# Kernel optimization log

Hardware: AMD Instinct MI355X
Metric: run time of the kernel (lower is better)

Reference implementation:

```python
import jax, jax.numpy as jnp
import numpy as np

N = 100000
E = 1600000
G = 64  # number of graphs
EPS = 1e-5
NEG_SLOPE = 0.2


def _gat_conv(x, W, a_src, a_dst, b, src, dst, n, H, C):
    # x: [n, in]; W: [in, H*C]; a_src/a_dst: [H, C]; b: [H*C]
    h = (x @ W).reshape(n, H, C)                      # [n,H,C]
    al_s = jnp.sum(h * a_src, axis=-1)                # [n,H]
    al_d = jnp.sum(h * a_dst, axis=-1)                # [n,H]
    score = jax.nn.leaky_relu(al_s[src] + al_d[dst], NEG_SLOPE)  # [E,H]
    # segment softmax over incoming edges of each dst node
    m = jax.ops.segment_max(score, dst, num_segments=n)
    ex = jnp.exp(score - jax.lax.stop_gradient(m)[dst])
    den = jax.ops.segment_sum(ex, dst, num_segments=n)
    alpha = ex / den[dst]                             # [E,H]
    out = jax.ops.segment_sum(alpha[:, :, None] * h[src], dst, num_segments=n)
    return out.reshape(n, H * C) + b


def _bn_relu(x, gamma, beta):
    mu = jnp.mean(x, axis=0)
    var = jnp.var(x, axis=0)  # biased, matches torch BN normalization
    return jax.nn.relu((x - mu) * jax.lax.rsqrt(var + EPS) * gamma + beta)


def setup_inputs() -> dict:
    key = jax.random.key(0)
    ks = jax.random.split(key, 32)
    d = {}
    d['x'] = jax.random.normal(ks[0], (N, 3), dtype=jnp.float32)
    d['edge_index'] = jax.random.randint(ks[1], (2, E), 0, N, dtype=jnp.int64)
    d['batch'] = jnp.sort(jax.random.randint(ks[2], (N,), 0, G, dtype=jnp.int64))
    def p(k, shape):
        return jax.random.normal(k, shape, dtype=jnp.float32) * 0.1
    # conv1: 3 -> 16, heads=2
    d['W1'] = p(ks[3], (3, 32)); d['as1'] = p(ks[4], (2, 16)); d['ad1'] = p(ks[5], (2, 16)); d['b1'] = p(ks[6], (32,))
    d['g1'] = jnp.ones((32,), jnp.float32); d['be1'] = jnp.zeros((32,), jnp.float32)
    # conv2: 32 -> 32, heads=2
    d['W2'] = p(ks[7], (32, 64)); d['as2'] = p(ks[8], (2, 32)); d['ad2'] = p(ks[9], (2, 32)); d['b2'] = p(ks[10], (64,))
    d['g2'] = jnp.ones((64,), jnp.float32); d['be2'] = jnp.zeros((64,), jnp.float32)
    # conv3: 64 -> 64, heads=2
    d['W3'] = p(ks[11], (64, 128)); d['as3'] = p(ks[12], (2, 64)); d['ad3'] = p(ks[13], (2, 64)); d['b3'] = p(ks[14], (128,))
    d['g3'] = jnp.ones((128,), jnp.float32); d['be3'] = jnp.zeros((128,), jnp.float32)
    d['fcw'] = p(ks[15], (128, 10)); d['fcb'] = p(ks[16], (10,))
    return d


def reference(x, edge_index, batch, W1, as1, ad1, b1, g1, be1, W2, as2, ad2, b2, g2, be2, W3, as3, ad3, b3, g3, be3, fcw, fcb):
    n = x.shape[0]
    loops = jnp.arange(n, dtype=edge_index.dtype)  # PyG GATConv add_self_loops=True
    src = jnp.concatenate([edge_index[0], loops])
    dst = jnp.concatenate([edge_index[1], loops])
    h = _bn_relu(_gat_conv(x, W1, as1, ad1, b1, src, dst, n, 2, 16), g1, be1)
    h = _bn_relu(_gat_conv(h, W2, as2, ad2, b2, src, dst, n, 2, 32), g2, be2)
    h = _bn_relu(_gat_conv(h, W3, as3, ad3, b3, src, dst, n, 2, 64), g3, be3)
    pooled = jax.ops.segment_max(h, batch, num_segments=G)  # [G,128]
    return pooled @ fcw + fcb
```

## Files before the change

kernel.cpp:

```cpp
#include <hip/hip_runtime.h>
#include <cstddef>

constexpr int NN = 100000;
constexpr int NE = 1600000;
constexpr int TE = NE + NN;
constexpr int NG = 64;
constexpr float EPS = 1e-5f;
constexpr float NEG_SLOPE = 0.2f;
constexpr int NREP = 16;

constexpr int NBUCK = 256;
constexpr int DPB = 391;
constexpr int PHB = 256;
constexpr int CH = (TE + PHB - 1) / PHB;

__device__ __forceinline__ unsigned short f2bf(float f) {
    unsigned u = __float_as_uint(f);
    u += 0x7fffu + ((u >> 16) & 1u);
    return (unsigned short)(u >> 16);
}
__device__ __forceinline__ float bf2f(unsigned short s) {
    return __uint_as_float((unsigned)s << 16);
}
__device__ __forceinline__ float bflo(unsigned u) { return __uint_as_float(u << 16); }
__device__ __forceinline__ float bfhi(unsigned u) { return __uint_as_float(u & 0xffff0000u); }
__device__ __forceinline__ void unpack8(uint4 v, float* f) {
    f[0] = bflo(v.x); f[1] = bfhi(v.x); f[2] = bflo(v.y); f[3] = bfhi(v.y);
    f[4] = bflo(v.z); f[5] = bfhi(v.z); f[6] = bflo(v.w); f[7] = bfhi(v.w);
}
__device__ __forceinline__ uint4 pack8(const float* o) {
    uint4 pk;
    pk.x = (unsigned)f2bf(o[0]) | ((unsigned)f2bf(o[1]) << 16);
    pk.y = (unsigned)f2bf(o[2]) | ((unsigned)f2bf(o[3]) << 16);
    pk.z = (unsigned)f2bf(o[4]) | ((unsigned)f2bf(o[5]) << 16);
    pk.w = (unsigned)f2bf(o[6]) | ((unsigned)f2bf(o[7]) << 16);
    return pk;
}
__device__ __forceinline__ float lrelu(float v) { return v > 0.f ? v : NEG_SLOPE * v; }


__global__ void k_hist(const int* __restrict__ ei, int* __restrict__ hist) {
    __shared__ int hcnt[NBUCK];
    for (int i = threadIdx.x; i < NBUCK; i += 256) hcnt[i] = 0;
    __syncthreads();
    int k = blockIdx.x;
    int e0 = k * CH, e1 = min(e0 + CH, TE);
    for (int e = e0 + threadIdx.x; e < e1; e += 256) {
        int d = (e < NE) ? ei[NE + e] : (e - NE);
        atomicAdd(&hcnt[d / DPB], 1);
    }
    __syncthreads();
    for (int b = threadIdx.x; b < NBUCK; b += 256) hist[b * PHB + k] = hcnt[b];
}

__global__ void k_scanA(int* __restrict__ hist, int* __restrict__ bsum) {
    __shared__ int ls[PHB];
    int b = blockIdx.x, t = threadIdx.x;
    int v = hist[b * PHB + t];
    ls[t] = v;
    __syncthreads();
    for (int off = 1; off < PHB; off <<= 1) {
        int add = (t >= off) ? ls[t - off] : 0;
        __syncthreads();
        ls[t] += add;
        __syncthreads();
    }
    hist[b * PHB + t] = ls[t] - v;
    if (t == PHB - 1) bsum[b] = ls[t];
}

__global__ void k_scanB(const int* __restrict__ bsum, int* __restrict__ bbase,
                        int* __restrict__ rowptr) {
    __shared__ int ls[NBUCK];
    int t = threadIdx.x;
    int v = bsum[t];
    ls[t] = v;
    __syncthreads();
    for (int off = 1; off < NBUCK; off <<= 1) {
        int add = (t >= off) ? ls[t - off] : 0;
        __syncthreads();
        ls[t] += add;
        __syncthreads();
    }
    bbase[t] = ls[t] - v;
    if (t == NBUCK - 1) { bbase[NBUCK] = ls[t]; rowptr[NN] = ls[t]; }
}

__global__ void k_scatter(const int* __restrict__ ei, const int* __restrict__ hist,
                          const int* __restrict__ bbase, int* __restrict__ pairs) {
    __shared__ int cur[NBUCK];
    int k = blockIdx.x;
    for (int b = threadIdx.x; b < NBUCK; b += 256) cur[b] = bbase[b] + hist[b * PHB + k];
    __syncthreads();
    int e0 = k * CH, e1 = min(e0 + CH, TE);
    for (int e = e0 + threadIdx.x; e < e1; e += 256) {
        int s, d;
        if (e < NE) { s = ei[e]; d = ei[NE + e]; } else { s = e - NE; d = s; }
        int b = d / DPB, ld = d - b * DPB;
        int pos = atomicAdd(&cur[b], 1);
        pairs[pos] = (s << 9) | ld;
    }
}

__global__ void k_csr(const int* __restrict__ pairs, const int* __restrict__ bbase,
                      int* __restrict__ rowptr, int* __restrict__ colsrc) {
    __shared__ int deg[DPB];
    __shared__ int exc[DPB];
    __shared__ int sc[512];
    int b = blockIdx.x, t = threadIdx.x;
    int base = bbase[b], cnt = bbase[b + 1] - base;
    int d0 = b * DPB;
    int ndst = min(DPB, NN - d0);
    for (int i = t; i < DPB; i += 256) deg[i] = 0;
    __syncthreads();
    for (int i = t; i < cnt; i += 256) atomicAdd(&deg[pairs[base + i] & 511], 1);
    __syncthreads();
    sc[t] = (t < DPB) ? deg[t] : 0;
    sc[t + 256] = (t + 256 < DPB) ? deg[t + 256] : 0;
    __syncthreads();
    for (int off = 1; off < 512; off <<= 1) {
        int a0 = (t >= off) ? sc[t - off] : 0;
        int a1 = (t + 256 >= off) ? sc[t + 256 - off] : 0;
        __syncthreads();
        sc[t] += a0; sc[t + 256] += a1;
        __syncthreads();
    }
    if (t < DPB) exc[t] = sc[t] - deg[t];
    if (t + 256 < DPB) exc[t + 256] = sc[t + 256] - deg[t + 256];
    __syncthreads();
    for (int i = t; i < ndst; i += 256) rowptr[d0 + i] = base + exc[i];
    for (int i = t; i < DPB; i += 256) deg[i] = 0;
    __syncthreads();
    for (int i = t; i < cnt; i += 256) {
        int p = pairs[base + i];
        int ld = p & 511;
        int s = (unsigned)p >> 9;
        int pos = base + exc[ld] + atomicAdd(&deg[ld], 1);
        colsrc[pos] = s;
    }
}


__global__ void k_wa(const float* __restrict__ W1, const float* __restrict__ as1,
                     const float* __restrict__ ad1,
                     const float* __restrict__ W2, const float* __restrict__ as2,
                     const float* __restrict__ ad2,
                     const float* __restrict__ W3, const float* __restrict__ as3,
                     const float* __restrict__ ad3,
                     float* __restrict__ was1, float* __restrict__ wad1,
                     float* __restrict__ was2, float* __restrict__ wad2,
                     float* __restrict__ was3, float* __restrict__ wad3) {
    int t = threadIdx.x;
    if (t < 6) {
        int h = t / 3, i = t % 3;
        float s = 0.f, d = 0.f;
        for (int c = 0; c < 16; ++c) {
            float w = W1[i * 32 + h * 16 + c];
            s += w * as1[h * 16 + c];
            d += w * ad1[h * 16 + c];
        }
        was1[t] = s; wad1[t] = d;
    }
    if (t < 64) {
        int h = t / 32, i = t % 32;
        float s = 0.f, d = 0.f;
        for (int c = 0; c < 32; ++c) {
            float w = W2[i * 64 + h * 32 + c];
            s += w * as2[h * 32 + c];
            d += w * ad2[h * 32 + c];
        }
        was2[t] = s; wad2[t] = d;
    }
    if (t < 128) {
        int h = t / 64, i = t % 64;
        float s = 0.f, d = 0.f;
        for (int c = 0; c < 64; ++c) {
            float w = W3[i * 128 + h * 64 + c];
            s += w * as3[h * 64 + c];
            d += w * ad3[h * 64 + c];
        }
        was3[t] = s; wad3[t] = d;
    }
}


__global__ void k_logits1(const float* __restrict__ x, const float* __restrict__ was,
                          const float* __restrict__ wad, float* __restrict__ als,
                          float* __restrict__ ald) {
    int n = blockIdx.x * 256 + threadIdx.x;
    if (n >= NN) return;
    float x0 = x[n * 3], x1 = x[n * 3 + 1], x2 = x[n * 3 + 2];
    als[n * 2 + 0] = x0 * was[0] + x1 * was[1] + x2 * was[2];
    als[n * 2 + 1] = x0 * was[3] + x1 * was[4] + x2 * was[5];
    ald[n * 2 + 0] = x0 * wad[0] + x1 * wad[1] + x2 * wad[2];
    ald[n * 2 + 1] = x0 * wad[3] + x1 * wad[4] + x2 * wad[5];
}


template <int IN>
__global__ void k_prep(const unsigned short* __restrict__ x,
                       const float* __restrict__ bnrep,
                       const float* __restrict__ gamma, const float* __restrict__ beta,
                       const float* __restrict__ was, const float* __restrict__ wad,
                       unsigned short* __restrict__ xbn,
                       float* __restrict__ als, float* __restrict__ ald) {
    constexpr int P = IN / 8;
    __shared__ float sbn[2 * IN];
    __shared__ float swa[4 * IN];
    if (threadIdx.x < IN) {
        int c = threadIdx.x;
        float s = 0.f, ss = 0.f;
#pragma unroll
        for (int r = 0; r < NREP; ++r) {
            s  += bnrep[r * 2 * IN + c];
            ss += bnrep[r * 2 * IN + IN + c];
        }
        float mu = s / NN;
        float var = ss / NN - mu * mu;
        float sca = gamma[c] * rsqrtf(var + EPS);
        sbn[c] = sca;
        sbn[IN + c] = beta[c] - mu * sca;
    }
    for (int i = threadIdx.x; i < 2 * IN; i += 256) {
        swa[i] = was[i];
        swa[2 * IN + i] = wad[i];
    }
    __syncthreads();
    int idx = blockIdx.x * 256 + threadIdx.x;
    int node = idx / P, pl = idx % P;
    if (node >= NN) return;
    uint4 v = *(const uint4*)&x[(size_t)node * IN + pl * 8];
    float f[8];
    unpack8(v, f);
    float s0 = 0.f, s1 = 0.f, d0 = 0.f, d1 = 0.f;
#pragma unroll
    for (int k = 0; k < 8; ++k) {
        int c = pl * 8 + k;
        float t = f[k] * sbn[c] + sbn[IN + c];
        t = t > 0.f ? t : 0.f;
        f[k] = t;
        s0 += t * swa[c];           s1 += t * swa[IN + c];
        d0 += t * swa[2 * IN + c];  d1 += t * swa[3 * IN + c];
    }
    *(uint4*)&xbn[(size_t)node * IN + pl * 8] = pack8(f);
#pragma unroll
    for (int m = 1; m < P; m <<= 1) {
        s0 += __shfl_xor(s0, m, 64); s1 += __shfl_xor(s1, m, 64);
        d0 += __shfl_xor(d0, m, 64); d1 += __shfl_xor(d1, m, 64);
    }
    if (pl == 0) {
        als[node * 2 + 0] = s0; als[node * 2 + 1] = s1;
        ald[node * 2 + 0] = d0; ald[node * 2 + 1] = d1;
    }
}


template <int IN>
__global__ void k_agg(const int* __restrict__ rowptr, const int* __restrict__ colsrc,
                      const unsigned short* __restrict__ x,
                      const float* __restrict__ als, const float* __restrict__ ald,
                      unsigned short* __restrict__ agg) {
    constexpr int LPE = IN / 8;
    constexpr int EPI2 = 32 / LPE;
    constexpr int UNR = 2;
    __shared__ float4 etab[4][64];
    int wv = threadIdx.x >> 6, lane = threadIdx.x & 63;
    int hw = lane >> 5, hl = lane & 31;
    int base = ((int)blockIdx.x * 4 + wv) * 2;
    int wid = base + hw;
    bool valid = wid < NN;
    int start = 0, cnt = 0;
    float2 dv = make_float2(0.f, 0.f);
    if (valid) {
        start = rowptr[wid];
        cnt = rowptr[wid + 1] - start;
        dv = ((const float2*)ald)[wid];
    }
    int mc = max(cnt, __shfl_xor(cnt, 32, 64));

    if (mc <= 32) {
        int e = start + hl;
        bool act = valid && (hl < cnt);
        int s = act ? colsrc[e] : 0;
        float2 av = act ? ((const float2*)als)[s] : make_float2(0.f, 0.f);
        float t0 = act ? lrelu(av.x + dv.x) : -1e30f;
        float t1 = act ? lrelu(av.y + dv.y) : -1e30f;
        float m0 = t0, m1 = t1;
#pragma unroll
        for (int off = 16; off; off >>= 1) {
            m0 = fmaxf(m0, __shfl_xor(m0, off, 32));
            m1 = fmaxf(m1, __shfl_xor(m1, off, 32));
        }
        float w0 = act ? __expf(t0 - m0) : 0.f;
        float w1 = act ? __expf(t1 - m1) : 0.f;
        float den0 = w0, den1 = w1;
#pragma unroll
        for (int off = 16; off; off >>= 1) {
            den0 += __shfl_xor(den0, off, 32);
            den1 += __shfl_xor(den1, off, 32);
        }
        float i0 = valid ? 1.f / den0 : 0.f;
        float i1 = valid ? 1.f / den1 : 0.f;
        etab[wv][lane] = make_float4(__int_as_float(s), w0 * i0, w1 * i1, 0.f);
        int sub = hl / LPE, cl = hl % LPE;
        float a0[8], a1[8];
#pragma unroll
        for (int k = 0; k < 8; ++k) { a0[k] = 0.f; a1[k] = 0.f; }
        if (valid) {
            int cm1 = cnt - 1;
            for (int j0 = 0; j0 < cnt; j0 += EPI2 * UNR) {
                float l0[UNR], l1[UNR];
                uint4 hv[UNR];
#pragma unroll
                for (int u = 0; u < UNR; ++u) {
                    int jj = j0 + u * EPI2 + sub;
                    int jc = min(jj, cm1);
                    float4 ed = etab[wv][hw * 32 + jc];
                    bool on = jj <= cm1;
                    l0[u] = on ? ed.y : 0.f;
                    l1[u] = on ? ed.z : 0.f;
                    hv[u] = *(const uint4*)&x[(size_t)__float_as_int(ed.x) * IN + cl * 8];
                }
#pragma unroll
                for (int u = 0; u < UNR; ++u) {
                    float f[8];
                    unpack8(hv[u], f);
#pragma unroll
                    for (int k = 0; k < 8; ++k) {
                        a0[k] += l0[u] * f[k];
                        a1[k] += l1[u] * f[k];
                    }
                }
            }
        }
#pragma unroll
        for (int m = LPE; m < 32; m <<= 1) {
#pragma unroll
            for (int k = 0; k < 8; ++k) {
                a0[k] += __shfl_xor(a0[k], m, 64);
                a1[k] += __shfl_xor(a1[k], m, 64);
            }
        }
        if (valid && sub == 0) {
            *(uint4*)&agg[(size_t)wid * 2 * IN + cl * 8] = pack8(a0);
            *(uint4*)&agg[(size_t)wid * 2 * IN + IN + cl * 8] = pack8(a1);
        }
    } else {
        for (int i2 = 0; i2 < 2; ++i2) {
            int w2 = base + i2;
            if (w2 >= NN) continue;
            int st = rowptr[w2], en = rowptr[w2 + 1];
            float2 dv2 = ((const float2*)ald)[w2];
            float m0 = -1e30f, m1 = -1e30f;
            for (int e = st + lane; e < en; e += 64) {
                int s = colsrc[e];
                m0 = fmaxf(m0, lrelu(als[s * 2 + 0] + dv2.x));
                m1 = fmaxf(m1, lrelu(als[s * 2 + 1] + dv2.y));
            }
#pragma unroll
            for (int off = 32; off; off >>= 1) {
                m0 = fmaxf(m0, __shfl_xor(m0, off, 64));
                m1 = fmaxf(m1, __shfl_xor(m1, off, 64));
            }
            float den0 = 0.f, den1 = 0.f;
            for (int e = st + lane; e < en; e += 64) {
                int s = colsrc[e];
                den0 += __expf(lrelu(als[s * 2 + 0] + dv2.x) - m0);
                den1 += __expf(lrelu(als[s * 2 + 1] + dv2.y) - m1);
            }
#pragma unroll
            for (int off = 32; off; off >>= 1) {
                den0 += __shfl_xor(den0, off, 64);
                den1 += __shfl_xor(den1, off, 64);
            }
            float inv0 = 1.f / den0, inv1 = 1.f / den1;
            int c = lane;
            float a0 = 0.f, a1 = 0.f;
            for (int e = st; e < en; ++e) {
                int s = colsrc[e];
                float aa0 = __expf(lrelu(als[s * 2 + 0] + dv2.x) - m0) * inv0;
                float aa1 = __expf(lrelu(als[s * 2 + 1] + dv2.y) - m1) * inv1;
                if (c < IN) {
                    float vv = bf2f(x[(size_t)s * IN + c]);
                    a0 += aa0 * vv;
                    a1 += aa1 * vv;
                }
            }
            if (c < IN) {
                agg[(size_t)w2 * 2 * IN + c] = f2bf(a0);
                agg[(size_t)w2 * 2 * IN + IN + c] = f2bf(a1);
            }
        }
    }
}

__global__ void k_agg1(const int* __restrict__ rowptr, const int* __restrict__ colsrc,
                       const float* __restrict__ x, const float* __restrict__ als,
                       const float* __restrict__ ald, float* __restrict__ agg) {
    int wv = threadIdx.x >> 6, lane = threadIdx.x & 63;
    int hw = lane >> 5, hl = lane & 31;
    int base = ((int)blockIdx.x * 4 + wv) * 2;
    int wid = base + hw;
    bool valid = wid < NN;
    int start = 0, cnt = 0;
    float2 dv = make_float2(0.f, 0.f);
    if (valid) {
        start = rowptr[wid];
        cnt = rowptr[wid + 1] - start;
        dv = ((const float2*)ald)[wid];
    }
    int mc = max(cnt, __shfl_xor(cnt, 32, 64));
    if (mc <= 32) {
        int e = start + hl;
        bool act = valid && (hl < cnt);
        int s = act ? colsrc[e] : 0;
        float2 av = act ? ((const float2*)als)[s] : make_float2(0.f, 0.f);
        float t0 = act ? lrelu(av.x + dv.x) : -1e30f;
        float t1 = act ? lrelu(av.y + dv.y) : -1e30f;
        float m0 = t0, m1 = t1;
#pragma unroll
        for (int off = 16; off; off >>= 1) {
            m0 = fmaxf(m0, __shfl_xor(m0, off, 32));
            m1 = fmaxf(m1, __shfl_xor(m1, off, 32));
        }
        float w0 = act ? __expf(t0 - m0) : 0.f;
        float w1 = act ? __expf(t1 - m1) : 0.f;
        float den0 = w0, den1 = w1;
#pragma unroll
        for (int off = 16; off; off >>= 1) {
            den0 += __shfl_xor(den0, off, 32);
            den1 += __shfl_xor(den1, off, 32);
        }
        float a[6];
#pragma unroll
        for (int k = 0; k < 6; ++k) a[k] = 0.f;
        if (act) {
            float al0 = w0 / den0, al1 = w1 / den1;
            float x0 = x[s * 3], x1 = x[s * 3 + 1], x2 = x[s * 3 + 2];
            a[0] = al0 * x0; a[1] = al0 * x1; a[2] = al0 * x2;
            a[3] = al1 * x0; a[4] = al1 * x1; a[5] = al1 * x2;
        }
#pragma unroll
        for (int m = 1; m < 32; m <<= 1) {
#pragma unroll
            for (int k = 0; k < 6; ++k) a[k] += __shfl_xor(a[k], m, 64);
        }
        if (valid && hl == 0) {
#pragma unroll
            for (int k = 0; k < 6; ++k) agg[(size_t)wid * 6 + k] = a[k];
        }
    } else {
        for (int i2 = 0; i2 < 2; ++i2) {
            int w2 = base + i2;
            if (w2 >= NN) continue;
            int st = rowptr[w2], en = rowptr[w2 + 1];
            float2 dv2 = ((const float2*)ald)[w2];
            float m0 = -1e30f, m1 = -1e30f;
            for (int e = st + lane; e < en; e += 64) {
                int s = colsrc[e];
                m0 = fmaxf(m0, lrelu(als[s * 2 + 0] + dv2.x));
                m1 = fmaxf(m1, lrelu(als[s * 2 + 1] + dv2.y));
            }
#pragma unroll
            for (int off = 32; off; off >>= 1) {
                m0 = fmaxf(m0, __shfl_xor(m0, off, 64));
                m1 = fmaxf(m1, __shfl_xor(m1, off, 64));
            }
            float den0 = 0.f, den1 = 0.f;
            for (int e = st + lane; e < en; e += 64) {
                int s = colsrc[e];
                den0 += __expf(lrelu(als[s * 2 + 0] + dv2.x) - m0);
                den1 += __expf(lrelu(als[s * 2 + 1] + dv2.y) - m1);
            }
#pragma unroll
            for (int off = 32; off; off >>= 1) {
                den0 += __shfl_xor(den0, off, 64);
                den1 += __shfl_xor(den1, off, 64);
            }
            float inv0 = 1.f / den0, inv1 = 1.f / den1;
            float a[6];
#pragma unroll
            for (int k = 0; k < 6; ++k) a[k] = 0.f;
            for (int e = st + lane; e < en; e += 64) {
                int s = colsrc[e];
                float aa0 = __expf(lrelu(als[s * 2 + 0] + dv2.x) - m0) * inv0;
                float aa1 = __expf(lrelu(als[s * 2 + 1] + dv2.y) - m1) * inv1;
                float x0 = x[s * 3], x1 = x[s * 3 + 1], x2 = x[s * 3 + 2];
                a[0] += aa0 * x0; a[1] += aa0 * x1; a[2] += aa0 * x2;
                a[3] += aa1 * x0; a[4] += aa1 * x1; a[5] += aa1 * x2;
            }
#pragma unroll
            for (int m = 1; m < 64; m <<= 1) {
#pragma unroll
                for (int k = 0; k < 6; ++k) a[k] += __shfl_xor(a[k], m, 64);
            }
            if (lane == 0) {
#pragma unroll
                for (int k = 0; k < 6; ++k) agg[(size_t)w2 * 6 + k] = a[k];
            }
        }
    }
}


template <int IN, int OUT, int GRP>
__global__ void k_transform(const unsigned short* __restrict__ agg,
                            const float* __restrict__ W,
                            unsigned short* __restrict__ xout,
                            float* __restrict__ bnrep, int n) {
    constexpr int TPN = OUT / 4;
    constexpr int NB = 256 / TPN;
    constexpr int NPAD = 2 * IN + 8;
    constexpr int HPAD = IN + 4;
    __shared__ float xs[GRP * NB * NPAD];
    __shared__ float red[2 * OUT];
    for (int i = threadIdx.x; i < 2 * OUT; i += 256) red[i] = 0.f;
    int node0 = blockIdx.x * GRP * NB;
    const unsigned* au = (const unsigned*)agg + (size_t)node0 * IN;
    for (int i = threadIdx.x; i < GRP * NB * IN; i += 256) {
        int nn = node0 + i / IN;
        unsigned u = (nn < n) ? au[i] : 0u;
        int cp = 2 * (i % IN);
        int lo = (cp < IN) ? cp : HPAD + (cp - IN);
        int b = (i / IN) * NPAD + lo;
        xs[b] = bflo(u);
        xs[b + 1] = bfhi(u);
    }
    __syncthreads();
    int nl = threadIdx.x / TPN, q = threadIdx.x % TPN;
    int hd = (q >= TPN / 2);
    float4 acc[GRP];
#pragma unroll
    for (int g = 0; g < GRP; ++g) acc[g] = make_float4(0.f, 0.f, 0.f, 0.f);
#pragma unroll 4
    for (int i = 0; i < IN; ++i) {
        float4 w = *(const float4*)&W[i * OUT + q * 4];
#pragma unroll
        for (int g = 0; g < GRP; ++g) {
            float xv = xs[(g * NB + nl) * NPAD + hd * HPAD + i];
            acc[g].x += xv * w.x; acc[g].y += xv * w.y;
            acc[g].z += xv * w.z; acc[g].w += xv * w.w;
        }
    }
    float s4[4] = {0.f, 0.f, 0.f, 0.f}, ss4[4] = {0.f, 0.f, 0.f, 0.f};
#pragma unroll
    for (int g = 0; g < GRP; ++g) {
        int node = node0 + g * NB + nl;
        if (node < n) {
            uint2 pk;
            pk.x = (unsigned)f2bf(acc[g].x) | ((unsigned)f2bf(acc[g].y) << 16);
            pk.y = (unsigned)f2bf(acc[g].z) | ((unsigned)f2bf(acc[g].w) << 16);
            *(uint2*)&xout[(size_t)node * OUT + q * 4] = pk;
            s4[0] += acc[g].x; s4[1] += acc[g].y; s4[2] += acc[g].z; s4[3] += acc[g].w;
            ss4[0] += acc[g].x * acc[g].x; ss4[1] += acc[g].y * acc[g].y;
            ss4[2] += acc[g].z * acc[g].z; ss4[3] += acc[g].w * acc[g].w;
        }
    }
#pragma unroll
    for (int k = 0; k < 4; ++k) {
        atomicAdd(&red[q * 4 + k], s4[k]);
        atomicAdd(&red[OUT + q * 4 + k], ss4[k]);
    }
    __syncthreads();
    float* dst = &bnrep[(blockIdx.x & (NREP - 1)) * 2 * OUT];
    for (int i = threadIdx.x; i < 2 * OUT; i += 256) atomicAdd(&dst[i], red[i]);
}

__global__ void k_transform1(const float* __restrict__ agg, const float* __restrict__ W,
                             unsigned short* __restrict__ xout, float* __restrict__ bnrep,
                             int n) {
    __shared__ float xs[32 * 7];
    __shared__ float red[64];
    for (int i = threadIdx.x; i < 64; i += 256) red[i] = 0.f;
    int node0 = blockIdx.x * 32;
    for (int i = threadIdx.x; i < 192; i += 256) {
        int nn = node0 + i / 6;
        float v = (nn < n) ? agg[(size_t)node0 * 6 + i] : 0.f;
        xs[(i / 6) * 7 + (i % 6)] = v;
    }
    __syncthreads();
    int nl = threadIdx.x / 8, q = threadIdx.x % 8;
    int hd = (q >= 4);
    int node = node0 + nl;
    float4 acc = {0.f, 0.f, 0.f, 0.f};
#pragma unroll
    for (int i = 0; i < 3; ++i) {
        float xv = xs[nl * 7 + hd * 3 + i];
        float4 w = *(const float4*)&W[i * 32 + q * 4];
        acc.x += xv * w.x; acc.y += xv * w.y; acc.z += xv * w.z; acc.w += xv * w.w;
    }
    if (node < n) {
        uint2 pk;
        pk.x = (unsigned)f2bf(acc.x) | ((unsigned)f2bf(acc.y) << 16);
        pk.y = (unsigned)f2bf(acc.z) | ((unsigned)f2bf(acc.w) << 16);
        *(uint2*)&xout[(size_t)node * 32 + q * 4] = pk;
        atomicAdd(&red[q * 4 + 0], acc.x); atomicAdd(&red[32 + q * 4 + 0], acc.x * acc.x);
        atomicAdd(&red[q * 4 + 1], acc.y); atomicAdd(&red[32 + q * 4 + 1], acc.y * acc.y);
        atomicAdd(&red[q * 4 + 2], acc.z); atomicAdd(&red[32 + q * 4 + 2], acc.z * acc.z);
        atomicAdd(&red[q * 4 + 3], acc.w); atomicAdd(&red[32 + q * 4 + 3], acc.w * acc.w);
    }
    __syncthreads();
    float* dst = &bnrep[(blockIdx.x & (NREP - 1)) * 64];
    for (int i = threadIdx.x; i < 64; i += 256) atomicAdd(&dst[i], red[i]);
}


__global__ void k_pool(const unsigned short* __restrict__ h, const int* __restrict__ batch,
                       const float* __restrict__ bnrep, const float* __restrict__ gamma,
                       const float* __restrict__ beta, float* __restrict__ pooled, int n) {
    const int K = 32;
    int c = threadIdx.x;
    float s = 0.f, ss = 0.f;
#pragma unroll
    for (int r = 0; r < NREP; ++r) {
        s  += bnrep[r * 256 + c];
        ss += bnrep[r * 256 + 128 + c];
    }
    float mu = s / n;
    float var = ss / n - mu * mu;
    float scale = gamma[c] * rsqrtf(var + EPS);
    float shift = beta[c] - mu * scale;
    int n0 = blockIdx.x * K;
    if (n0 >= n) return;
    int nend = min(n, n0 + K);
    int curg = batch[n0];
    float m = 0.f;
    for (int nn = n0; nn < nend; ++nn) {
        int g = batch[nn];
        if (g != curg) {
            atomicMax((int*)&pooled[curg * 128 + c], __float_as_int(m));
            m = 0.f; curg = g;
        }
        float v = bf2f(h[(size_t)nn * 128 + c]) * scale + shift;
        m = fmaxf(m, v > 0.f ? v : 0.f);
    }
    atomicMax((int*)&pooled[curg * 128 + c], __float_as_int(m));
}

__global__ void k_fc(const float* __restrict__ pooled, const float* __restrict__ fcw,
                     const float* __restrict__ fcb, float* __restrict__ out) {
    int t = threadIdx.x;
    if (t >= NG * 10) return;
    int g = t / 10, j = t % 10;
    float acc = fcb[j];
#pragma unroll
    for (int c = 0; c < 128; ++c) acc += pooled[g * 128 + c] * fcw[c * 10 + j];
    out[g * 10 + j] = acc;
}


extern "C" void kernel_launch(void* const* d_in, const int* in_sizes, int n_in,
                              void* d_out, int out_size, void* d_ws, size_t ws_size,
                              hipStream_t stream) {
    const float* x   = (const float*)d_in[0];
    const int*   ei  = (const int*)d_in[1];
    const int*   bat = (const int*)d_in[2];
    const float* W1  = (const float*)d_in[3];
    const float* as1 = (const float*)d_in[4];
    const float* ad1 = (const float*)d_in[5];
    const float* g1  = (const float*)d_in[7];
    const float* be1 = (const float*)d_in[8];
    const float* W2  = (const float*)d_in[9];
    const float* as2 = (const float*)d_in[10];
    const float* ad2 = (const float*)d_in[11];
    const float* g2  = (const float*)d_in[13];
    const float* be2 = (const float*)d_in[14];
    const float* W3  = (const float*)d_in[15];
    const float* as3 = (const float*)d_in[16];
    const float* ad3 = (const float*)d_in[17];
    const float* g3  = (const float*)d_in[19];
    const float* be3 = (const float*)d_in[20];
    const float* fcw = (const float*)d_in[21];
    const float* fcb = (const float*)d_in[22];
    float* out = (float*)d_out;

    char* w = (char*)d_ws;
    size_t off = 0;
    auto take = [&](size_t bytes) {
        void* p = w + off;
        off += (bytes + 255) & ~(size_t)255;
        return p;
    };
    constexpr size_t ZN = (size_t)NREP * 2 * (32 + 64 + 128) + NG * 128;
    char* zreg = (char*)take(ZN * 4);
    float* bnr1   = (float*)zreg;
    float* bnr2   = bnr1 + NREP * 64;
    float* bnr3   = bnr2 + NREP * 128;
    float* pooled = bnr3 + NREP * 256;

    int*   hist    = (int*)take((size_t)NBUCK * PHB * 4);
    int*   bsum    = (int*)take(NBUCK * 4);
    int*   bbase   = (int*)take((NBUCK + 1) * 4);
    int*   rowptr  = (int*)take((size_t)(NN + 1) * 4);
    int*   pairs   = (int*)take((size_t)TE * 4);
    int*   colsrc  = (int*)take((size_t)TE * 4);
    float* al_s    = (float*)take((size_t)NN * 2 * 4);
    float* al_d    = (float*)take((size_t)NN * 2 * 4);
    float* was1    = (float*)take(64);
    float* wad1    = (float*)take(64);
    float* was2    = (float*)take(64 * 4);
    float* wad2    = (float*)take(64 * 4);
    float* was3    = (float*)take(128 * 4);
    float* wad3    = (float*)take(128 * 4);
    float* agg1f   = (float*)take((size_t)NN * 6 * 4);
    unsigned short* aggb = (unsigned short*)take((size_t)NN * 128 * 2);
    unsigned short* x2   = (unsigned short*)take((size_t)NN * 32 * 2);
    unsigned short* xbn2 = (unsigned short*)take((size_t)NN * 32 * 2);
    unsigned short* x3   = (unsigned short*)take((size_t)NN * 64 * 2);
    unsigned short* xbn3 = (unsigned short*)take((size_t)NN * 64 * 2);
    unsigned short* x4   = (unsigned short*)take((size_t)NN * 128 * 2);

    hipMemsetAsync(zreg, 0, ZN * 4, stream);

    k_hist<<<PHB, 256, 0, stream>>>(ei, hist);
    k_scanA<<<NBUCK, PHB, 0, stream>>>(hist, bsum);
    k_scanB<<<1, NBUCK, 0, stream>>>(bsum, bbase, rowptr);
    k_scatter<<<PHB, 256, 0, stream>>>(ei, hist, bbase, pairs);
    k_csr<<<NBUCK, 256, 0, stream>>>(pairs, bbase, rowptr, colsrc);

    k_wa<<<1, 256, 0, stream>>>(W1, as1, ad1, W2, as2, ad2, W3, as3, ad3,
                                was1, wad1, was2, wad2, was3, wad3);

    const int AGG_BLOCKS = (NN + 7) / 8;

    k_logits1<<<(NN + 255) / 256, 256, 0, stream>>>(x, was1, wad1, al_s, al_d);
    k_agg1<<<AGG_BLOCKS, 256, 0, stream>>>(rowptr, colsrc, x, al_s, al_d, agg1f);
    k_transform1<<<(NN + 31) / 32, 256, 0, stream>>>(agg1f, W1, x2, bnr1, NN);

    k_prep<32><<<(NN * 4 + 255) / 256, 256, 0, stream>>>(x2, bnr1, g1, be1, was2, wad2,
                                                         xbn2, al_s, al_d);
    k_agg<32><<<AGG_BLOCKS, 256, 0, stream>>>(rowptr, colsrc, xbn2, al_s, al_d, aggb);
    k_transform<32, 64, 4><<<(NN + 63) / 64, 256, 0, stream>>>(aggb, W2, x3, bnr2, NN);

    k_prep<64><<<(NN * 8 + 255) / 256, 256, 0, stream>>>(x3, bnr2, g2, be2, was3, wad3,
                                                         xbn3, al_s, al_d);
    k_agg<64><<<AGG_BLOCKS, 256, 0, stream>>>(rowptr, colsrc, xbn3, al_s, al_d, aggb);
    k_transform<64, 128, 4><<<(NN + 31) / 32, 256, 0, stream>>>(aggb, W3, x4, bnr3, NN);

    k_pool<<<(NN + 31) / 32, 128, 0, stream>>>(x4, bat, bnr3, g3, be3, pooled, NN);
    k_fc<<<1, 640, 0, stream>>>(pooled, fcw, fcb, out);
}
```

Baseline: 374.4 us.

## Use bf16 MFMA with hi/lo split weights for layer 2/3 transforms

Replaces the scalar FMA shared-memory transform kernels for conv2 and conv3 with an MFMA kernel (16x16x32 bf16). Weights are pre-split into bf16 high and low parts by a new small kernel, so the fp32 weights keep near-fp32 precision at the cost of two MFMAs per step. The new kernel loads the aggregated bf16 activations straight into registers and no longer stages them in shared memory, while the per-channel BN statistics are still reduced through shared-memory atomics. It relies on NN being a multiple of 32, since it has no bounds checks, and writes outputs as scattered 2-byte stores.

```diff
diff --git a/kernel.cpp b/kernel.cpp
--- a/kernel.cpp
+++ b/kernel.cpp
@@ -14,6 +14,9 @@
 constexpr int PHB = 256;
 constexpr int CH = (TE + PHB - 1) / PHB;
 
+typedef __attribute__((ext_vector_type(8))) short bf16x8;
+typedef __attribute__((ext_vector_type(4))) float f32x4;
+
 __device__ __forceinline__ unsigned short f2bf(float f) {
     unsigned u = __float_as_uint(f);
     u += 0x7fffu + ((u >> 16) & 1u);
@@ -35,6 +38,11 @@
     pk.z = (unsigned)f2bf(o[4]) | ((unsigned)f2bf(o[5]) << 16);
     pk.w = (unsigned)f2bf(o[6]) | ((unsigned)f2bf(o[7]) << 16);
     return pk;
+}
+__device__ __forceinline__ bf16x8 ld_bf8(const unsigned short* p) {
+    union { uint4 u; bf16x8 b; } cv;
+    cv.u = *(const uint4*)p;
+    return cv.b;
 }
 __device__ __forceinline__ float lrelu(float v) { return v > 0.f ? v : NEG_SLOPE * v; }
 
@@ -180,6 +188,29 @@
             d += w * ad3[h * 64 + c];
         }
         was3[t] = s; wad3[t] = d;
+    }
+}
+
+
+__global__ void k_wsplit(const float* __restrict__ W2, const float* __restrict__ W3,
+                         unsigned short* __restrict__ w2hi, unsigned short* __restrict__ w2lo,
+                         unsigned short* __restrict__ w3hi, unsigned short* __restrict__ w3lo) {
+    int t = blockIdx.x * 256 + threadIdx.x;
+    if (t < 2048) {
+        int c = t / 32, i = t % 32;
+        float w = W2[i * 64 + c];
+        unsigned short hi = f2bf(w);
+        float lo = w - bf2f(hi);
+        w2hi[c * 32 + i] = hi;
+        w2lo[c * 32 + i] = f2bf(lo);
+    }
+    if (t < 8192) {
+        int c = t / 64, i = t % 64;
+        float w = W3[i * 128 + c];
+        unsigned short hi = f2bf(w);
+        float lo = w - bf2f(hi);
+        w3hi[c * 64 + i] = hi;
+        w3lo[c * 64 + i] = f2bf(lo);
     }
 }
 
@@ -503,63 +534,53 @@
 }
 
 
-template <int IN, int OUT, int GRP>
-__global__ void k_transform(const unsigned short* __restrict__ agg,
-                            const float* __restrict__ W,
-                            unsigned short* __restrict__ xout,
-                            float* __restrict__ bnrep, int n) {
-    constexpr int TPN = OUT / 4;
-    constexpr int NB = 256 / TPN;
-    constexpr int NPAD = 2 * IN + 8;
-    constexpr int HPAD = IN + 4;
-    __shared__ float xs[GRP * NB * NPAD];
+template <int IN, int OUT>
+__global__ void k_tmfma(const unsigned short* __restrict__ agg,
+                        const unsigned short* __restrict__ whi,
+                        const unsigned short* __restrict__ wlo,
+                        unsigned short* __restrict__ xout,
+                        float* __restrict__ bnrep) {
+    constexpr int C = OUT / 2;
+    constexpr int NT = C / 16;
+    constexpr int KS = IN / 32;
     __shared__ float red[2 * OUT];
     for (int i = threadIdx.x; i < 2 * OUT; i += 256) red[i] = 0.f;
-    int node0 = blockIdx.x * GRP * NB;
-    const unsigned* au = (const unsigned*)agg + (size_t)node0 * IN;
-    for (int i = threadIdx.x; i < GRP * NB * IN; i += 256) {
-        int nn = node0 + i / IN;
-        unsigned u = (nn < n) ? au[i] : 0u;
-        int cp = 2 * (i % IN);
-        int lo = (cp < IN) ? cp : HPAD + (cp - IN);
-        int b = (i / IN) * NPAD + lo;
-        xs[b] = bflo(u);
-        xs[b + 1] = bfhi(u);
-    }
-    __syncthreads();
-    int nl = threadIdx.x / TPN, q = threadIdx.x % TPN;
-    int hd = (q >= TPN / 2);
-    float4 acc[GRP];
-#pragma unroll
-    for (int g = 0; g < GRP; ++g) acc[g] = make_float4(0.f, 0.f, 0.f, 0.f);
-#pragma unroll 4
-    for (int i = 0; i < IN; ++i) {
-        float4 w = *(const float4*)&W[i * OUT + q * 4];
-#pragma unroll
-        for (int g = 0; g < GRP; ++g) {
-            float xv = xs[(g * NB + nl) * NPAD + hd * HPAD + i];
-            acc[g].x += xv * w.x; acc[g].y += xv * w.y;
-            acc[g].z += xv * w.z; acc[g].w += xv * w.w;
-        }
-    }
-    float s4[4] = {0.f, 0.f, 0.f, 0.f}, ss4[4] = {0.f, 0.f, 0.f, 0.f};
-#pragma unroll
-    for (int g = 0; g < GRP; ++g) {
-        int node = node0 + g * NB + nl;
-        if (node < n) {
-            uint2 pk;
-            pk.x = (unsigned)f2bf(acc[g].x) | ((unsigned)f2bf(acc[g].y) << 16);
-            pk.y = (unsigned)f2bf(acc[g].z) | ((unsigned)f2bf(acc[g].w) << 16);
-            *(uint2*)&xout[(size_t)node * OUT + q * 4] = pk;
-            s4[0] += acc[g].x; s4[1] += acc[g].y; s4[2] += acc[g].z; s4[3] += acc[g].w;
-            ss4[0] += acc[g].x * acc[g].x; ss4[1] += acc[g].y * acc[g].y;
-            ss4[2] += acc[g].z * acc[g].z; ss4[3] += acc[g].w * acc[g].w;
-        }
-    }
-#pragma unroll
-    for (int k = 0; k < 4; ++k) {
-        atomicAdd(&red[q * 4 + k], s4[k]);
-        atomicAdd(&red[OUT + q * 4 + k], ss4[k]);
+    __syncthreads();
+    int wv = threadIdx.x >> 6, l = threadIdx.x & 63;
+    int head = wv & 1;
+    int node0 = blockIdx.x * 32 + (wv >> 1) * 16;
+    int lr = l & 15, kg = l >> 4;
+    bf16x8 a[KS];
+#pragma unroll
+    for (int ks = 0; ks < KS; ++ks)
+        a[ks] = ld_bf8(&agg[(size_t)(node0 + lr) * 2 * IN + head * IN + ks * 32 + kg * 8]);
+    f32x4 acc[NT];
+#pragma unroll
+    for (int nt = 0; nt < NT; ++nt) acc[nt] = (f32x4){0.f, 0.f, 0.f, 0.f};
+#pragma unroll
+    for (int nt = 0; nt < NT; ++nt) {
+        int ch = head * C + nt * 16 + lr;
+#pragma unroll
+        for (int ks = 0; ks < KS; ++ks) {
+            bf16x8 bh = ld_bf8(&whi[(size_t)ch * IN + ks * 32 + kg * 8]);
+            bf16x8 bl = ld_bf8(&wlo[(size_t)ch * IN + ks * 32 + kg * 8]);
+            acc[nt] = __builtin_amdgcn_mfma_f32_16x16x32_bf16(a[ks], bh, acc[nt], 0, 0, 0);
+            acc[nt] = __builtin_amdgcn_mfma_f32_16x16x32_bf16(a[ks], bl, acc[nt], 0, 0, 0);
+        }
+    }
+#pragma unroll
+    for (int nt = 0; nt < NT; ++nt) {
+        int chO = head * C + nt * 16 + lr;
+        float s = 0.f, ss = 0.f;
+#pragma unroll
+        for (int r = 0; r < 4; ++r) {
+            float v = acc[nt][r];
+            int node = node0 + kg * 4 + r;
+            xout[(size_t)node * OUT + chO] = f2bf(v);
+            s += v; ss += v * v;
+        }
+        atomicAdd(&red[chO], s);
+        atomicAdd(&red[OUT + chO], ss);
     }
     __syncthreads();
     float* dst = &bnrep[(blockIdx.x & (NREP - 1)) * 2 * OUT];
@@ -702,6 +723,10 @@
     float* wad2    = (float*)take(64 * 4);
     float* was3    = (float*)take(128 * 4);
     float* wad3    = (float*)take(128 * 4);
+    unsigned short* w2hi = (unsigned short*)take(2048 * 2);
+    unsigned short* w2lo = (unsigned short*)take(2048 * 2);
+    unsigned short* w3hi = (unsigned short*)take(8192 * 2);
+    unsigned short* w3lo = (unsigned short*)take(8192 * 2);
     float* agg1f   = (float*)take((size_t)NN * 6 * 4);
     unsigned short* aggb = (unsigned short*)take((size_t)NN * 128 * 2);
     unsigned short* x2   = (unsigned short*)take((size_t)NN * 32 * 2);
@@ -720,6 +745,7 @@
 
     k_wa<<<1, 256, 0, stream>>>(W1, as1, ad1, W2, as2, ad2, W3, as3, ad3,
                                 was1, wad1, was2, wad2, was3, wad3);
+    k_wsplit<<<32, 256, 0, stream>>>(W2, W3, w2hi, w2lo, w3hi, w3lo);
 
     const int AGG_BLOCKS = (NN + 7) / 8;
 
@@ -730,12 +756,12 @@
     k_prep<32><<<(NN * 4 + 255) / 256, 256, 0, stream>>>(x2, bnr1, g1, be1, was2, wad2,
                                                          xbn2, al_s, al_d);
     k_agg<32><<<AGG_BLOCKS, 256, 0, stream>>>(rowptr, colsrc, xbn2, al_s, al_d, aggb);
-    k_transform<32, 64, 4><<<(NN + 63) / 64, 256, 0, stream>>>(aggb, W2, x3, bnr2, NN);
+    k_tmfma<32, 64><<<NN / 32, 256, 0, stream>>>(aggb, w2hi, w2lo, x3, bnr2);
 
     k_prep<64><<<(NN * 8 + 255) / 256, 256, 0, stream>>>(x3, bnr2, g2, be2, was3, wad3,
                                                          xbn3, al_s, al_d);
     k_agg<64><<<AGG_BLOCKS, 256, 0, stream>>>(rowptr, colsrc, xbn3, al_s, al_d, aggb);
-    k_transform<64, 128, 4><<<(NN + 31) / 32, 256, 0, stream>>>(aggb, W3, x4, bnr3, NN);
+    k_tmfma<64, 128><<<NN / 32, 256, 0, stream>>>(aggb, w3hi, w3lo, x4, bnr3);
 
     k_pool<<<(NN + 31) / 32, 128, 0, stream>>>(x4, bat, bnr3, g3, be3, pooled, NN);
     k_fc<<<1, 640, 0, stream>>>(pooled, fcw, fcb, out);
```

Result: faster. 349.8 us, median of 2 (-6.6%).
